# Optimization experiments

Measured on AMD Instinct MI355X. Metric: run time of the kernel, lower is better.

Reference implementation:

```python
import jax, jax.numpy as jnp
import numpy as np

BINS = 2048
SCENE = 8
EPS = 1e-8
P_LOW = 2.0
P_HIGH = 100.0


def setup_inputs() -> dict:
    key = jax.random.key(0)
    k1, k2 = jax.random.split(key)
    x = jax.random.uniform(k1, (8, 1, 1024, 1280), dtype=jnp.float32)
    delta = jax.random.normal(k2, (SCENE, BINS), dtype=jnp.float32)
    return {"x": x, "delta": delta}


def reference(x, delta):
    B = x.shape[0]
    if x.shape[1] == 3:
        x = jnp.mean(x, axis=1, keepdims=True)
    # robust per-sample quantile normalization -> [0, 1]
    x_flat = x.reshape(B, -1)
    lo = jnp.quantile(x_flat, P_LOW / 100.0, axis=1).reshape(B, 1, 1, 1)
    hi = jnp.quantile(x_flat, P_HIGH / 100.0, axis=1).reshape(B, 1, 1, 1)
    xn = jnp.clip((x - lo) / (hi - lo + EPS), 0.0, 1.0)
    # uniform scene mixture (scene selector unused in original forward)
    scene_idx = jnp.ones((B, SCENE), dtype=x.dtype) / SCENE
    increments = jax.nn.softplus(scene_idx @ delta) + EPS  # (B, BINS)
    luts = jnp.cumsum(increments, axis=1)
    luts = luts / (luts[:, -1:] + EPS) * 2.0 - 1.0  # monotonic, range ~[-1, 1]
    # per-sample gather: pixel value -> bin index -> LUT value
    idx = jnp.clip((xn * (BINS - 1)).astype(jnp.int32), 0, BINS - 1)  # (B,1,H,W)
    y = jnp.take_along_axis(luts, idx.reshape(B, -1), axis=1).reshape(xn.shape)
    return jnp.tile(y, (1, 3, 1, 1))
```

## Files before the change

### kernel.cpp

```cpp
#include <hip/hip_runtime.h>
#include <hip/hip_bf16.h>
#include <math.h>

#define NB 8
#define HH 1024
#define WW 1280
#define HW (HH*WW)
#define N4 (HW/4)
#define LBINS 2048
#define HBINS 2048
#define NSCENE 8
#define EPSF 1e-8f
#define CAPMAX 8192
#define HBLK 64

typedef float f32x4 __attribute__((ext_vector_type(4)));

#define WS_PART    0
#define WS_PMAX    (WS_PART + NB*HBLK*HBINS)
#define WS_INFO    (WS_PMAX + NB*HBLK)
#define WS_LOHI    (WS_INFO + NB*4)
#define WS_LUT     (WS_LOHI + NB*2)
#define WS_CNT     (WS_LUT + LBINS)
#define WS_COLLECT (WS_CNT + NB)

__device__ __forceinline__ unsigned fkey(float f) {
    unsigned u = __float_as_uint(f);
    return (u & 0x80000000u) ? ~u : (u | 0x80000000u);
}
__device__ __forceinline__ float keyf(unsigned k) {
    unsigned u = (k & 0x80000000u) ? (k & 0x7fffffffu) : ~k;
    return __uint_as_float(u);
}

__global__ __launch_bounds__(256) void k_hist(const float* __restrict__ x,
                                              unsigned* __restrict__ ws) {
    __shared__ unsigned lh[HBINS];
    __shared__ float redf[4];
    const int s = blockIdx.y;
    for (int i = threadIdx.x; i < HBINS; i += 256) lh[i] = 0u;
    __syncthreads();
    const float4* xs = (const float4*)(x + (size_t)s * HW);
    float mx = -3.4e38f;
    for (int i = blockIdx.x * 256 + threadIdx.x; i < N4; i += HBLK * 256) {
        float4 v = xs[i];
        float fv[4] = {v.x, v.y, v.z, v.w};
#pragma unroll
        for (int c = 0; c < 4; ++c) {
            float f = fv[c];
            int b = (int)(f * 2048.0f);
            b = b < 0 ? 0 : (b > 2047 ? 2047 : b);
            atomicAdd(&lh[b], 1u);
            mx = fmaxf(mx, f);
        }
    }
    for (int d = 32; d > 0; d >>= 1) mx = fmaxf(mx, __shfl_down(mx, d));
    if ((threadIdx.x & 63) == 0) redf[threadIdx.x >> 6] = mx;
    __syncthreads();
    unsigned* myp = ws + WS_PART + ((size_t)s * HBLK + blockIdx.x) * HBINS;
    for (int i = threadIdx.x; i < HBINS; i += 256) myp[i] = lh[i];
    if (threadIdx.x == 0) {
        float m2 = fmaxf(fmaxf(redf[0], redf[1]), fmaxf(redf[2], redf[3]));
        ((float*)(ws + WS_PMAX))[s * HBLK + blockIdx.x] = m2;
    }
}

__global__ __launch_bounds__(256) void k_scan_lut(unsigned* __restrict__ ws,
                                                  const float* __restrict__ delta) {
    __shared__ unsigned su[256];
    __shared__ float sf[256];
    const int s = blockIdx.x;
    const int tid = threadIdx.x;
    if (s == NB) {
        float inc[8];
        float run = 0.0f;
#pragma unroll
        for (int i = 0; i < 8; ++i) {
            int j = tid * 8 + i;
            float ssum = 0.0f;
#pragma unroll
            for (int sc = 0; sc < NSCENE; ++sc) ssum += delta[sc * LBINS + j];
            float v = ssum * 0.125f;
            run += fmaxf(v, 0.0f) + log1pf(expf(-fabsf(v))) + EPSF;
            inc[i] = run;
        }
        sf[tid] = run;
        __syncthreads();
        for (int d = 1; d < 256; d <<= 1) {
            float add = (tid >= d) ? sf[tid - d] : 0.0f;
            __syncthreads();
            sf[tid] += add;
            __syncthreads();
        }
        float excl = sf[tid] - run;
        float total = sf[255];
        float* lut = (float*)(ws + WS_LUT);
#pragma unroll
        for (int i = 0; i < 8; ++i)
            lut[tid * 8 + i] = (excl + inc[i]) / (total + EPSF) * 2.0f - 1.0f;
        return;
    }
    const unsigned* part = ws + WS_PART + (size_t)s * HBLK * HBINS;
    unsigned cnt[8];
    unsigned run = 0u;
#pragma unroll
    for (int i = 0; i < 8; ++i) {
        int j = tid * 8 + i;
        unsigned c = 0;
        for (int b = 0; b < HBLK; ++b) c += part[b * HBINS + j];
        cnt[i] = c;
        run += c;
    }
    su[tid] = run;
    __syncthreads();
    for (int d = 1; d < 256; d <<= 1) {
        unsigned add = (tid >= d) ? su[tid - d] : 0u;
        __syncthreads();
        su[tid] += add;
        __syncthreads();
    }
    unsigned before = su[tid] - run;
    const float idxf = 0.02f * (float)(HW - 1);
    const unsigned k = (unsigned)idxf;
#pragma unroll
    for (int i = 0; i < 8; ++i) {
        unsigned c = cnt[i];
        unsigned bin = tid * 8 + i;
        if (before <= k && k < before + c) {
            ws[WS_INFO + s * 4 + 0] = bin;
            ws[WS_INFO + s * 4 + 2] = k - before;
        }
        if (before <= k + 1 && k + 1 < before + c) {
            ws[WS_INFO + s * 4 + 1] = bin;
        }
        before += c;
    }
    if (tid < 64) {
        float mx = ((const float*)(ws + WS_PMAX))[s * HBLK + tid];
        for (int d = 32; d > 0; d >>= 1) mx = fmaxf(mx, __shfl_down(mx, d));
        if (tid == 0) {
            ((float*)(ws + WS_LOHI))[s * 2 + 1] = mx;
            ws[WS_CNT + s] = 0u;
        }
    }
}

__global__ __launch_bounds__(256) void k_collect(const float* __restrict__ x,
                                                 unsigned* __restrict__ ws, int cap) {
    const int s = blockIdx.y;
    const unsigned t1 = ws[WS_INFO + s * 4 + 0];
    const unsigned t2 = ws[WS_INFO + s * 4 + 1];
    float* coll = (float*)(ws + WS_COLLECT) + (size_t)s * cap;
    unsigned* cnt = ws + WS_CNT + s;
    const float4* xs = (const float4*)(x + (size_t)s * HW);
    for (int i = blockIdx.x * 256 + threadIdx.x; i < N4; i += gridDim.x * 256) {
        float4 v = xs[i];
        float fv[4] = {v.x, v.y, v.z, v.w};
#pragma unroll
        for (int c = 0; c < 4; ++c) {
            float f = fv[c];
            int b = (int)(f * 2048.0f);
            b = b < 0 ? 0 : (b > 2047 ? 2047 : b);
            if ((unsigned)b >= t1 && (unsigned)b <= t2) {
                unsigned p = atomicAdd(cnt, 1u);
                if (p < (unsigned)cap) coll[p] = f;
            }
        }
    }
}

__global__ __launch_bounds__(256) void k_select(unsigned* __restrict__ ws, int cap) {
    __shared__ unsigned keys[CAPMAX];
    __shared__ unsigned hist[256];
    __shared__ unsigned pfx[256];
    __shared__ unsigned s_bucket, s_r;
    __shared__ unsigned s_L, s_E, s_mg;
    const int s = blockIdx.x;
    const int tid = threadIdx.x;
    unsigned m = ws[WS_CNT + s];
    if (m > (unsigned)cap) m = (unsigned)cap;
    const float* coll = (const float*)(ws + WS_COLLECT) + (size_t)s * cap;
    const unsigned jrel = ws[WS_INFO + s * 4 + 2];

    for (unsigned i = tid; i < m; i += 256) keys[i] = fkey(coll[i]);
    if (tid == 0) { s_L = 0; s_E = 0; s_mg = 0xFFFFFFFFu; }
    __syncthreads();

    unsigned prefix = 0;
    unsigned r = jrel;
    for (int shift = 24; shift >= 0; shift -= 8) {
        hist[tid] = 0u;
        __syncthreads();
        for (unsigned i = tid; i < m; i += 256) {
            unsigned kk = keys[i];
            bool ok = (shift == 24) || ((kk >> (shift + 8)) == prefix);
            if (ok) atomicAdd(&hist[(kk >> shift) & 255u], 1u);
        }
        __syncthreads();
        if (tid < 64) {
            unsigned a0 = hist[tid*4+0], a1 = hist[tid*4+1];
            unsigned a2 = hist[tid*4+2], a3 = hist[tid*4+3];
            unsigned sum = a0 + a1 + a2 + a3;
            unsigned inc = sum;
            for (int d = 1; d < 64; d <<= 1) {
                unsigned y = __shfl_up(inc, d);
                if (tid >= d) inc += y;
            }
            unsigned excl = inc - sum;
            pfx[tid*4+0] = excl;
            pfx[tid*4+1] = excl + a0;
            pfx[tid*4+2] = excl + a0 + a1;
            pfx[tid*4+3] = excl + a0 + a1 + a2;
        }
        __syncthreads();
        {
            unsigned e = pfx[tid], c = hist[tid];
            if (e <= r && r < e + c) { s_bucket = tid; s_r = r - e; }
        }
        __syncthreads();
        prefix = (prefix << 8) | s_bucket;
        r = s_r;
        __syncthreads();
    }
    const unsigned vk = prefix;
    unsigned lL = 0, lE = 0, lmg = 0xFFFFFFFFu;
    for (unsigned i = tid; i < m; i += 256) {
        unsigned kk = keys[i];
        lL += (kk < vk) ? 1u : 0u;
        lE += (kk == vk) ? 1u : 0u;
        if (kk > vk && kk < lmg) lmg = kk;
    }
    atomicAdd(&s_L, lL);
    atomicAdd(&s_E, lE);
    atomicMin(&s_mg, lmg);
    __syncthreads();
    if (tid == 0) {
        unsigned vk1 = (jrel + 1 < s_L + s_E) ? vk : s_mg;
        float svk = keyf(vk), svk1 = keyf(vk1);
        const float idxf = 0.02f * (float)(HW - 1);
        const float frac = idxf - (float)((unsigned)idxf);
        ((float*)(ws + WS_LOHI))[s * 2 + 0] = svk * (1.0f - frac) + svk1 * frac;
    }
}

__global__ __launch_bounds__(256) void k_apply(const float* __restrict__ x,
                                               const unsigned* __restrict__ ws,
                                               float* __restrict__ y) {
    __shared__ float slut[LBINS];
    const float* lutg = (const float*)(ws + WS_LUT);
    for (int i = threadIdx.x; i < LBINS; i += 256) slut[i] = lutg[i];
    const int s = blockIdx.y;
    const float* lh = (const float*)(ws + WS_LOHI);
    const float lo = lh[s * 2 + 0];
    const float hi = lh[s * 2 + 1];
    const float denom = hi - lo + EPSF;
    __syncthreads();
    const f32x4* xs = (const f32x4*)(x + (size_t)s * HW);
    f32x4* y0 = (f32x4*)(y + (size_t)s * 3 * HW);
    f32x4* y1 = (f32x4*)(y + (size_t)s * 3 * HW + HW);
    f32x4* y2 = (f32x4*)(y + (size_t)s * 3 * HW + 2 * HW);
    for (int i = blockIdx.x * 256 + threadIdx.x; i < N4; i += gridDim.x * 256) {
        f32x4 v = xs[i];
        f32x4 o;
#pragma unroll
        for (int c = 0; c < 4; ++c) {
            float xn = (v[c] - lo) / denom;
            xn = xn < 0.0f ? 0.0f : (xn > 1.0f ? 1.0f : xn);
            float t = xn * 2047.0f;
            int idx = (int)t;
            idx = idx < 0 ? 0 : (idx > 2047 ? 2047 : idx);
            o[c] = slut[idx];
        }
        __builtin_nontemporal_store(o, &y0[i]);
        __builtin_nontemporal_store(o, &y1[i]);
        __builtin_nontemporal_store(o, &y2[i]);
    }
}

extern "C" void kernel_launch(void* const* d_in, const int* in_sizes, int n_in,
                              void* d_out, int out_size, void* d_ws, size_t ws_size,
                              hipStream_t stream) {
    const float* x = (const float*)d_in[0];
    const float* delta = (const float*)d_in[1];
    float* y = (float*)d_out;
    unsigned* ws = (unsigned*)d_ws;

    int cap = CAPMAX;
    size_t avail_words = ws_size / 4;
    size_t per_sample = avail_words > WS_COLLECT ? (avail_words - WS_COLLECT) / NB : 0;
    if ((size_t)cap > per_sample) cap = (int)per_sample;

    k_hist<<<dim3(HBLK, NB), dim3(256), 0, stream>>>(x, ws);
    k_scan_lut<<<dim3(NB + 1), dim3(256), 0, stream>>>(ws, delta);
    k_collect<<<dim3(64, NB), dim3(256), 0, stream>>>(x, ws, cap);
    k_select<<<dim3(NB), dim3(256), 0, stream>>>(ws, cap);
    k_apply<<<dim3(320, NB), dim3(256), 0, stream>>>(x, ws, y);
}
```

Measured before the change: 298.0 us.

## Fuse histogram, scan, collect and select into one cooperative kernel

Merges the four statistics kernels (histogram, scan/LUT build, candidate collection, radix select) into a single cooperative launch of 512 blocks, using grid-wide syncs between phases instead of separate kernel launches. This removes three launch boundaries and their gaps. In exchange it adds grid.sync barriers and raises static shared memory to about 34 KB per block. Phases that use only a few blocks, such as the scan and select, leave the other blocks idle at the barriers.

```diff
diff --git a/kernel.cpp b/kernel.cpp
--- a/kernel.cpp
+++ b/kernel.cpp
@@ -1,6 +1,9 @@
 #include <hip/hip_runtime.h>
 #include <hip/hip_bf16.h>
+#include <hip/hip_cooperative_groups.h>
 #include <math.h>
+
+namespace cg = cooperative_groups;
 
 #define NB 8
 #define HH 1024
@@ -13,6 +16,7 @@
 #define EPSF 1e-8f
 #define CAPMAX 8192
 #define HBLK 64
+#define SGRID (NB*HBLK)
 
 typedef float f32x4 __attribute__((ext_vector_type(4)));
 
@@ -33,45 +37,48 @@
     return __uint_as_float(u);
 }
 
-__global__ __launch_bounds__(256) void k_hist(const float* __restrict__ x,
-                                              unsigned* __restrict__ ws) {
-    __shared__ unsigned lh[HBINS];
-    __shared__ float redf[4];
-    const int s = blockIdx.y;
-    for (int i = threadIdx.x; i < HBINS; i += 256) lh[i] = 0u;
-    __syncthreads();
-    const float4* xs = (const float4*)(x + (size_t)s * HW);
-    float mx = -3.4e38f;
-    for (int i = blockIdx.x * 256 + threadIdx.x; i < N4; i += HBLK * 256) {
-        float4 v = xs[i];
-        float fv[4] = {v.x, v.y, v.z, v.w};
-#pragma unroll
-        for (int c = 0; c < 4; ++c) {
-            float f = fv[c];
-            int b = (int)(f * 2048.0f);
-            b = b < 0 ? 0 : (b > 2047 ? 2047 : b);
-            atomicAdd(&lh[b], 1u);
-            mx = fmaxf(mx, f);
-        }
-    }
-    for (int d = 32; d > 0; d >>= 1) mx = fmaxf(mx, __shfl_down(mx, d));
-    if ((threadIdx.x & 63) == 0) redf[threadIdx.x >> 6] = mx;
-    __syncthreads();
-    unsigned* myp = ws + WS_PART + ((size_t)s * HBLK + blockIdx.x) * HBINS;
-    for (int i = threadIdx.x; i < HBINS; i += 256) myp[i] = lh[i];
-    if (threadIdx.x == 0) {
-        float m2 = fmaxf(fmaxf(redf[0], redf[1]), fmaxf(redf[2], redf[3]));
-        ((float*)(ws + WS_PMAX))[s * HBLK + blockIdx.x] = m2;
-    }
-}
-
-__global__ __launch_bounds__(256) void k_scan_lut(unsigned* __restrict__ ws,
-                                                  const float* __restrict__ delta) {
-    __shared__ unsigned su[256];
-    __shared__ float sf[256];
-    const int s = blockIdx.x;
+__global__ __launch_bounds__(256) void k_stats(const float* __restrict__ x,
+                                               const float* __restrict__ delta,
+                                               unsigned* __restrict__ ws, int cap) {
+    cg::grid_group grid = cg::this_grid();
+    __shared__ unsigned smem[8709];
     const int tid = threadIdx.x;
-    if (s == NB) {
+    const int s64 = blockIdx.x >> 6;
+    const int b64 = blockIdx.x & 63;
+
+    {
+        unsigned* lh = smem;
+        float* redf = (float*)(smem + HBINS);
+        for (int i = tid; i < HBINS; i += 256) lh[i] = 0u;
+        __syncthreads();
+        const float4* xs = (const float4*)(x + (size_t)s64 * HW);
+        float mx = -3.4e38f;
+        for (int i = b64 * 256 + tid; i < N4; i += HBLK * 256) {
+            float4 v = xs[i];
+            float fv[4] = {v.x, v.y, v.z, v.w};
+#pragma unroll
+            for (int c = 0; c < 4; ++c) {
+                float f = fv[c];
+                int b = (int)(f * 2048.0f);
+                b = b < 0 ? 0 : (b > 2047 ? 2047 : b);
+                atomicAdd(&lh[b], 1u);
+                mx = fmaxf(mx, f);
+            }
+        }
+        for (int d = 32; d > 0; d >>= 1) mx = fmaxf(mx, __shfl_down(mx, d));
+        if ((tid & 63) == 0) redf[tid >> 6] = mx;
+        __syncthreads();
+        unsigned* myp = ws + WS_PART + ((size_t)s64 * HBLK + b64) * HBINS;
+        for (int i = tid; i < HBINS; i += 256) myp[i] = lh[i];
+        if (tid == 0) {
+            float m2 = fmaxf(fmaxf(redf[0], redf[1]), fmaxf(redf[2], redf[3]));
+            ((float*)(ws + WS_PMAX))[s64 * HBLK + b64] = m2;
+        }
+    }
+    grid.sync();
+
+    if (blockIdx.x == NB) {
+        float* sf = (float*)smem;
         float inc[8];
         float run = 0.0f;
 #pragma unroll
@@ -98,148 +105,148 @@
 #pragma unroll
         for (int i = 0; i < 8; ++i)
             lut[tid * 8 + i] = (excl + inc[i]) / (total + EPSF) * 2.0f - 1.0f;
-        return;
-    }
-    const unsigned* part = ws + WS_PART + (size_t)s * HBLK * HBINS;
-    unsigned cnt[8];
-    unsigned run = 0u;
-#pragma unroll
-    for (int i = 0; i < 8; ++i) {
-        int j = tid * 8 + i;
-        unsigned c = 0;
-        for (int b = 0; b < HBLK; ++b) c += part[b * HBINS + j];
-        cnt[i] = c;
-        run += c;
-    }
-    su[tid] = run;
-    __syncthreads();
-    for (int d = 1; d < 256; d <<= 1) {
-        unsigned add = (tid >= d) ? su[tid - d] : 0u;
-        __syncthreads();
-        su[tid] += add;
-        __syncthreads();
-    }
-    unsigned before = su[tid] - run;
-    const float idxf = 0.02f * (float)(HW - 1);
-    const unsigned k = (unsigned)idxf;
-#pragma unroll
-    for (int i = 0; i < 8; ++i) {
-        unsigned c = cnt[i];
-        unsigned bin = tid * 8 + i;
-        if (before <= k && k < before + c) {
-            ws[WS_INFO + s * 4 + 0] = bin;
-            ws[WS_INFO + s * 4 + 2] = k - before;
-        }
-        if (before <= k + 1 && k + 1 < before + c) {
-            ws[WS_INFO + s * 4 + 1] = bin;
-        }
-        before += c;
-    }
-    if (tid < 64) {
-        float mx = ((const float*)(ws + WS_PMAX))[s * HBLK + tid];
-        for (int d = 32; d > 0; d >>= 1) mx = fmaxf(mx, __shfl_down(mx, d));
-        if (tid == 0) {
-            ((float*)(ws + WS_LOHI))[s * 2 + 1] = mx;
-            ws[WS_CNT + s] = 0u;
-        }
-    }
-}
-
-__global__ __launch_bounds__(256) void k_collect(const float* __restrict__ x,
-                                                 unsigned* __restrict__ ws, int cap) {
-    const int s = blockIdx.y;
-    const unsigned t1 = ws[WS_INFO + s * 4 + 0];
-    const unsigned t2 = ws[WS_INFO + s * 4 + 1];
-    float* coll = (float*)(ws + WS_COLLECT) + (size_t)s * cap;
-    unsigned* cnt = ws + WS_CNT + s;
-    const float4* xs = (const float4*)(x + (size_t)s * HW);
-    for (int i = blockIdx.x * 256 + threadIdx.x; i < N4; i += gridDim.x * 256) {
-        float4 v = xs[i];
-        float fv[4] = {v.x, v.y, v.z, v.w};
-#pragma unroll
-        for (int c = 0; c < 4; ++c) {
-            float f = fv[c];
-            int b = (int)(f * 2048.0f);
-            b = b < 0 ? 0 : (b > 2047 ? 2047 : b);
-            if ((unsigned)b >= t1 && (unsigned)b <= t2) {
-                unsigned p = atomicAdd(cnt, 1u);
-                if (p < (unsigned)cap) coll[p] = f;
-            }
-        }
-    }
-}
-
-__global__ __launch_bounds__(256) void k_select(unsigned* __restrict__ ws, int cap) {
-    __shared__ unsigned keys[CAPMAX];
-    __shared__ unsigned hist[256];
-    __shared__ unsigned pfx[256];
-    __shared__ unsigned s_bucket, s_r;
-    __shared__ unsigned s_L, s_E, s_mg;
-    const int s = blockIdx.x;
-    const int tid = threadIdx.x;
-    unsigned m = ws[WS_CNT + s];
-    if (m > (unsigned)cap) m = (unsigned)cap;
-    const float* coll = (const float*)(ws + WS_COLLECT) + (size_t)s * cap;
-    const unsigned jrel = ws[WS_INFO + s * 4 + 2];
-
-    for (unsigned i = tid; i < m; i += 256) keys[i] = fkey(coll[i]);
-    if (tid == 0) { s_L = 0; s_E = 0; s_mg = 0xFFFFFFFFu; }
-    __syncthreads();
-
-    unsigned prefix = 0;
-    unsigned r = jrel;
-    for (int shift = 24; shift >= 0; shift -= 8) {
-        hist[tid] = 0u;
-        __syncthreads();
+    } else if (blockIdx.x < NB) {
+        const int s = blockIdx.x;
+        unsigned* su = smem;
+        const unsigned* part = ws + WS_PART + (size_t)s * HBLK * HBINS;
+        unsigned cnt[8];
+        unsigned run = 0u;
+#pragma unroll
+        for (int i = 0; i < 8; ++i) {
+            int j = tid * 8 + i;
+            unsigned c = 0;
+            for (int b = 0; b < HBLK; ++b) c += part[b * HBINS + j];
+            cnt[i] = c;
+            run += c;
+        }
+        su[tid] = run;
+        __syncthreads();
+        for (int d = 1; d < 256; d <<= 1) {
+            unsigned add = (tid >= d) ? su[tid - d] : 0u;
+            __syncthreads();
+            su[tid] += add;
+            __syncthreads();
+        }
+        unsigned before = su[tid] - run;
+        const float idxf = 0.02f * (float)(HW - 1);
+        const unsigned k = (unsigned)idxf;
+#pragma unroll
+        for (int i = 0; i < 8; ++i) {
+            unsigned c = cnt[i];
+            unsigned bin = tid * 8 + i;
+            if (before <= k && k < before + c) {
+                ws[WS_INFO + s * 4 + 0] = bin;
+                ws[WS_INFO + s * 4 + 2] = k - before;
+            }
+            if (before <= k + 1 && k + 1 < before + c) {
+                ws[WS_INFO + s * 4 + 1] = bin;
+            }
+            before += c;
+        }
+        if (tid < 64) {
+            float mx = ((const float*)(ws + WS_PMAX))[s * HBLK + tid];
+            for (int d = 32; d > 0; d >>= 1) mx = fmaxf(mx, __shfl_down(mx, d));
+            if (tid == 0) {
+                ((float*)(ws + WS_LOHI))[s * 2 + 1] = mx;
+                ws[WS_CNT + s] = 0u;
+            }
+        }
+    }
+    grid.sync();
+
+    {
+        const unsigned t1 = ws[WS_INFO + s64 * 4 + 0];
+        const unsigned t2 = ws[WS_INFO + s64 * 4 + 1];
+        float* coll = (float*)(ws + WS_COLLECT) + (size_t)s64 * cap;
+        unsigned* cnt = ws + WS_CNT + s64;
+        const float4* xs = (const float4*)(x + (size_t)s64 * HW);
+        for (int i = b64 * 256 + tid; i < N4; i += HBLK * 256) {
+            float4 v = xs[i];
+            float fv[4] = {v.x, v.y, v.z, v.w};
+#pragma unroll
+            for (int c = 0; c < 4; ++c) {
+                float f = fv[c];
+                int b = (int)(f * 2048.0f);
+                b = b < 0 ? 0 : (b > 2047 ? 2047 : b);
+                if ((unsigned)b >= t1 && (unsigned)b <= t2) {
+                    unsigned p = atomicAdd(cnt, 1u);
+                    if (p < (unsigned)cap) coll[p] = f;
+                }
+            }
+        }
+    }
+    grid.sync();
+
+    if (blockIdx.x < NB) {
+        const int s = blockIdx.x;
+        unsigned* keys = smem;
+        unsigned* hist = smem + CAPMAX;
+        unsigned* pfx  = smem + CAPMAX + 256;
+        unsigned* sc   = smem + CAPMAX + 512;
+        unsigned m = ws[WS_CNT + s];
+        if (m > (unsigned)cap) m = (unsigned)cap;
+        const float* coll = (const float*)(ws + WS_COLLECT) + (size_t)s * cap;
+        const unsigned jrel = ws[WS_INFO + s * 4 + 2];
+
+        for (unsigned i = tid; i < m; i += 256) keys[i] = fkey(coll[i]);
+        if (tid == 0) { sc[2] = 0; sc[3] = 0; sc[4] = 0xFFFFFFFFu; }
+        __syncthreads();
+
+        unsigned prefix = 0;
+        unsigned r = jrel;
+        for (int shift = 24; shift >= 0; shift -= 8) {
+            hist[tid] = 0u;
+            __syncthreads();
+            for (unsigned i = tid; i < m; i += 256) {
+                unsigned kk = keys[i];
+                bool ok = (shift == 24) || ((kk >> (shift + 8)) == prefix);
+                if (ok) atomicAdd(&hist[(kk >> shift) & 255u], 1u);
+            }
+            __syncthreads();
+            if (tid < 64) {
+                unsigned a0 = hist[tid*4+0], a1 = hist[tid*4+1];
+                unsigned a2 = hist[tid*4+2], a3 = hist[tid*4+3];
+                unsigned sum = a0 + a1 + a2 + a3;
+                unsigned incv = sum;
+                for (int d = 1; d < 64; d <<= 1) {
+                    unsigned y = __shfl_up(incv, d);
+                    if (tid >= d) incv += y;
+                }
+                unsigned excl = incv - sum;
+                pfx[tid*4+0] = excl;
+                pfx[tid*4+1] = excl + a0;
+                pfx[tid*4+2] = excl + a0 + a1;
+                pfx[tid*4+3] = excl + a0 + a1 + a2;
+            }
+            __syncthreads();
+            {
+                unsigned e = pfx[tid], c = hist[tid];
+                if (e <= r && r < e + c) { sc[0] = tid; sc[1] = r - e; }
+            }
+            __syncthreads();
+            prefix = (prefix << 8) | sc[0];
+            r = sc[1];
+            __syncthreads();
+        }
+        const unsigned vk = prefix;
+        unsigned lL = 0, lE = 0, lmg = 0xFFFFFFFFu;
         for (unsigned i = tid; i < m; i += 256) {
             unsigned kk = keys[i];
-            bool ok = (shift == 24) || ((kk >> (shift + 8)) == prefix);
-            if (ok) atomicAdd(&hist[(kk >> shift) & 255u], 1u);
-        }
-        __syncthreads();
-        if (tid < 64) {
-            unsigned a0 = hist[tid*4+0], a1 = hist[tid*4+1];
-            unsigned a2 = hist[tid*4+2], a3 = hist[tid*4+3];
-            unsigned sum = a0 + a1 + a2 + a3;
-            unsigned inc = sum;
-            for (int d = 1; d < 64; d <<= 1) {
-                unsigned y = __shfl_up(inc, d);
-                if (tid >= d) inc += y;
-            }
-            unsigned excl = inc - sum;
-            pfx[tid*4+0] = excl;
-            pfx[tid*4+1] = excl + a0;
-            pfx[tid*4+2] = excl + a0 + a1;
-            pfx[tid*4+3] = excl + a0 + a1 + a2;
-        }
-        __syncthreads();
-        {
-            unsigned e = pfx[tid], c = hist[tid];
-            if (e <= r && r < e + c) { s_bucket = tid; s_r = r - e; }
-        }
-        __syncthreads();
-        prefix = (prefix << 8) | s_bucket;
-        r = s_r;
-        __syncthreads();
-    }
-    const unsigned vk = prefix;
-    unsigned lL = 0, lE = 0, lmg = 0xFFFFFFFFu;
-    for (unsigned i = tid; i < m; i += 256) {
-        unsigned kk = keys[i];
-        lL += (kk < vk) ? 1u : 0u;
-        lE += (kk == vk) ? 1u : 0u;
-        if (kk > vk && kk < lmg) lmg = kk;
-    }
-    atomicAdd(&s_L, lL);
-    atomicAdd(&s_E, lE);
-    atomicMin(&s_mg, lmg);
-    __syncthreads();
-    if (tid == 0) {
-        unsigned vk1 = (jrel + 1 < s_L + s_E) ? vk : s_mg;
-        float svk = keyf(vk), svk1 = keyf(vk1);
-        const float idxf = 0.02f * (float)(HW - 1);
-        const float frac = idxf - (float)((unsigned)idxf);
-        ((float*)(ws + WS_LOHI))[s * 2 + 0] = svk * (1.0f - frac) + svk1 * frac;
+            lL += (kk < vk) ? 1u : 0u;
+            lE += (kk == vk) ? 1u : 0u;
+            if (kk > vk && kk < lmg) lmg = kk;
+        }
+        atomicAdd(&sc[2], lL);
+        atomicAdd(&sc[3], lE);
+        atomicMin(&sc[4], lmg);
+        __syncthreads();
+        if (tid == 0) {
+            unsigned vk1 = (jrel + 1 < sc[2] + sc[3]) ? vk : sc[4];
+            float svk = keyf(vk), svk1 = keyf(vk1);
+            const float idxf = 0.02f * (float)(HW - 1);
+            const float frac = idxf - (float)((unsigned)idxf);
+            ((float*)(ws + WS_LOHI))[s * 2 + 0] = svk * (1.0f - frac) + svk1 * frac;
+        }
     }
 }
 
@@ -290,9 +297,8 @@
     size_t per_sample = avail_words > WS_COLLECT ? (avail_words - WS_COLLECT) / NB : 0;
     if ((size_t)cap > per_sample) cap = (int)per_sample;
 
-    k_hist<<<dim3(HBLK, NB), dim3(256), 0, stream>>>(x, ws);
-    k_scan_lut<<<dim3(NB + 1), dim3(256), 0, stream>>>(ws, delta);
-    k_collect<<<dim3(64, NB), dim3(256), 0, stream>>>(x, ws, cap);
-    k_select<<<dim3(NB), dim3(256), 0, stream>>>(ws, cap);
+    void* args[] = {(void*)&x, (void*)&delta, (void*)&ws, (void*)&cap};
+    hipLaunchCooperativeKernel((const void*)k_stats, dim3(SGRID), dim3(256),
+                               args, 0, stream);
     k_apply<<<dim3(320, NB), dim3(256), 0, stream>>>(x, ws, y);
 }
```

New measurement: 478.1 us. +60.4%, slower.
